# Kernel optimization log

Hardware: AMD Instinct MI355X
Metric: run time of the kernel (lower is better)

The kernel has to match this reference:

```python
import jax, jax.numpy as jnp
import numpy as np

N = 100_000   # nodes
E = 1_600_000 # edges (COO, directed as given)
D = 128       # input feature dim
H = 128       # hidden dim
L = 3         # layers


def setup_inputs() -> dict:
    key = jax.random.key(0)
    ks = jax.random.split(key, 2 + 2 * L)
    x = jax.random.normal(ks[0], (N, D), dtype=jnp.float32)
    edge_index = jax.random.randint(ks[1], (2, E), 0, N, dtype=jnp.int32)
    inp = {"x": x, "edge_index": edge_index}
    dims = [(D, H), (H, H), (H, H)]
    for i, (fi, fo) in enumerate(dims):
        scale = 1.0 / np.sqrt(fi)
        inp[f"W{i}"] = jax.random.uniform(ks[2 + 2 * i], (fi, fo), jnp.float32, -scale, scale)
        inp[f"b{i}"] = jax.random.uniform(ks[3 + 2 * i], (fo,), jnp.float32, -scale, scale)
    return inp


def reference(x, edge_index, W0, b0, W1, b1, W2, b2):
    n = x.shape[0]
    src, dst = edge_index[0], edge_index[1]
    # GCNConv default: add self-loops, symmetric D^{-1/2}(A+I)D^{-1/2} normalization
    loop = jnp.arange(n, dtype=edge_index.dtype)
    src = jnp.concatenate([src, loop])
    dst = jnp.concatenate([dst, loop])
    ones = jnp.ones(src.shape[0], dtype=x.dtype)
    deg = jax.ops.segment_sum(ones, dst, num_segments=n)          # [N]
    dinv = jnp.where(deg > 0, jax.lax.rsqrt(deg), 0.0)            # deg^{-1/2}, inf->0
    norm = dinv[src] * dinv[dst]                                  # [E+N]

    def gcn_conv(h, W, b):
        h = h @ W                                  # linear transform first (PyG order)
        msg = h[src] * norm[:, None]               # gather + scale, [E+N, H]
        return jax.ops.segment_sum(msg, dst, num_segments=n) + b

    for W, b in ((W0, b0), (W1, b1), (W2, b2)):
        x = jax.nn.relu(gcn_conv(x, W, b))
    return x
```

## Files before the change

kernel.cpp:

```cpp
#include <hip/hip_runtime.h>
#include <hip/hip_bf16.h>

#define TPB 256

typedef short s8v __attribute__((ext_vector_type(8)));
typedef float f4v __attribute__((ext_vector_type(4)));
typedef _Float16 h8v __attribute__((ext_vector_type(8)));

#define PB 128
#define BSHIFT 10
#define BSPAN 1024
#define PCHUNK 4096
#define WBLK 192
#define CAP 20480

__device__ __forceinline__ void split_f16(float v, _Float16& hi, _Float16& lo) {
    hi = (_Float16)v;
    lo = (_Float16)(v - (float)hi);
}


__global__ __launch_bounds__(256) void prep_kernel(const int* __restrict__ src,
                                                   const int* __restrict__ dst, int E,
                                                   int* __restrict__ bcursor,
                                                   unsigned int* __restrict__ part,
                                                   const float* __restrict__ W0,
                                                   const float* __restrict__ W1,
                                                   const float* __restrict__ W2,
                                                   unsigned short* __restrict__ Whi,
                                                   unsigned short* __restrict__ Wlo) {
    __shared__ int h[PB];
    __shared__ int gofs[PB];
    int t = threadIdx.x;
    if (blockIdx.x < WBLK) {
        int idx0 = blockIdx.x * 256 + t;
        if (idx0 < 3 * 16384) {
            int layer = idx0 >> 14;
            int e = idx0 & 16383;
            int k = e >> 7, ncol = e & 127;
            const float* W = (layer == 0) ? W0 : (layer == 1) ? W1 : W2;
            _Float16 hi, lo;
            split_f16(W[e], hi, lo);
            int ct = ncol >> 4;
            int lane = (((k >> 3) & 3) << 4) | (ncol & 15);
            int kki = k >> 5;
            int j = k & 7;
            int oidx = layer * 16384 + (((ct * 4 + kki) * 64 + lane) * 8 + j);
            ((_Float16*)Whi)[oidx] = hi;
            ((_Float16*)Wlo)[oidx] = lo;
        }
        return;
    }
    long base = (long)(blockIdx.x - WBLK) * PCHUNK;
    int cnt = (int)min((long)PCHUNK, (long)E - base);

    if (t < PB) h[t] = 0;
    __syncthreads();
    for (int j = t; j < cnt; j += 256)
        atomicAdd(&h[dst[base + j] >> BSHIFT], 1);
    __syncthreads();
    if (t < PB) {
        int c = h[t];
        int resv = (c > 0) ? atomicAdd(&bcursor[t], c) : 0;
        if (resv > CAP) resv = CAP;
        gofs[t] = t * CAP + resv;
    }
    __syncthreads();
    if (t < PB) h[t] = 0;
    __syncthreads();
    for (int j = t; j < cnt; j += 256) {
        int s = src[base + j], d = dst[base + j];
        int b = d >> BSHIFT;
        int idx = atomicAdd(&h[b], 1);
        long w = (long)gofs[b] + idx;
        long lim = (long)(b + 1) * CAP;
        if (w >= lim) w = lim - 1;
        part[w] = (unsigned int)s | ((unsigned int)(d & (BSPAN - 1)) << 17);
    }
}


__global__ __launch_bounds__(1024) void csr_kernel(const unsigned int* __restrict__ part,
                                                   const int* __restrict__ bcursor,
                                                   int* __restrict__ row, float* __restrict__ dinv,
                                                   int* __restrict__ esrc, int n, int E) {
    __shared__ int deg[BSPAN];
    __shared__ int lrow[BSPAN];
    __shared__ int cur[BSPAN];
    __shared__ int wsum[16];
    __shared__ int sbase[PB];
    __shared__ int wtot2[2];
    int b = blockIdx.x;
    int n0 = b << BSHIFT;
    int nn = min(BSPAN, n - n0);
    if (nn <= 0) return;
    int t = threadIdx.x;
    int lane = t & 63, wid = t >> 6;

    int szb = 0, v0 = 0;
    if (t < PB) {
        szb = min(bcursor[t], CAP);
        v0 = szb;
        for (int off = 1; off < 64; off <<= 1) {
            int u = __shfl_up(v0, off);
            if (lane >= off) v0 += u;
        }
        if (lane == 63) wtot2[wid] = v0;
    }
    __syncthreads();
    if (t < PB) {
        if (wid == 1) v0 += wtot2[0];
        sbase[t] = v0 - szb;
    }
    if (b == 0 && t == 0) row[n] = E;
    __syncthreads();
    int e0g = sbase[b];
    int size = min(bcursor[b], CAP);
    long pb0 = (long)b * CAP;

    deg[t] = 0;
    __syncthreads();
    for (int e = t; e < size; e += 1024)
        atomicAdd(&deg[part[pb0 + e] >> 17], 1);
    __syncthreads();

    int a = deg[t];
    int v = a;
    for (int off = 1; off < 64; off <<= 1) {
        int u = __shfl_up(v, off);
        if (lane >= off) v += u;
    }
    if (lane == 63) wsum[wid] = v;
    __syncthreads();
    if (wid == 0 && lane < 16) {
        int w = wsum[lane];
        for (int off = 1; off < 16; off <<= 1) {
            int u = __shfl_up(w, off);
            if (lane >= off) w += u;
        }
        wsum[lane] = w;
    }
    __syncthreads();
    int excl = v - a + ((wid > 0) ? wsum[wid - 1] : 0);
    lrow[t] = excl;
    cur[t] = 0;
    if (t < nn) {
        row[n0 + t] = e0g + excl;
        dinv[n0 + t] = rsqrtf((float)(deg[t] + 1));
    }
    __syncthreads();

    for (int e = t; e < size; e += 1024) {
        unsigned int p = part[pb0 + e];
        int d = p >> 17;
        int idx = atomicAdd(&cur[d], 1);
        esrc[e0g + lrow[d] + idx] = (int)(p & 0x1FFFFu);
    }
}


__global__ __launch_bounds__(256, 3) void gemm0_mfma(const float* __restrict__ Xf,
                                                     const unsigned short* __restrict__ Whs,
                                                     const unsigned short* __restrict__ Wls,
                                                     const float* __restrict__ dinv,
                                                     _Float16* __restrict__ Ch, int n) {
    __shared__ _Float16 Oh[128 * 136];
    int t = threadIdx.x;
    int wave = t >> 6, lane = t & 63;
    int ch = wave & 1, rh = wave >> 1;
    int lm = lane & 15, q = lane >> 4;
    long row0 = (long)blockIdx.x * 128 + rh * 64;

    const h8v* Wh8 = (const h8v*)Whs;
    const h8v* Wl8 = (const h8v*)Wls;

    float scs[4];
#pragma unroll
    for (int rt = 0; rt < 4; rt++) {
        long r = row0 + rt * 16 + lm;
        long rc = (r < n) ? r : (n - 1);
        scs[rt] = dinv[rc];
    }

    f4v acc[4][4];
#pragma unroll
    for (int rt = 0; rt < 4; rt++)
#pragma unroll
        for (int ct = 0; ct < 4; ct++) acc[rt][ct] = (f4v)0.0f;

#pragma unroll
    for (int kki = 0; kki < 4; kki++) {
        h8v bh[4], bl[4];
#pragma unroll
        for (int ct = 0; ct < 4; ct++) {
            int idx = (((ch * 4 + ct) * 4 + kki) * 64) + lane;
            bh[ct] = Wh8[idx];
            bl[ct] = Wl8[idx];
        }
        h8v ah[4], al[4];
#pragma unroll
        for (int rt = 0; rt < 4; rt++) {
            long r = row0 + rt * 16 + lm;
            long rr = (r < n) ? r : (n - 1);
            const float4* xf4 = (const float4*)(Xf + rr * 128 + kki * 32 + q * 8);
            float4 u0 = xf4[0], u1 = xf4[1];
            float uf[8] = {u0.x, u0.y, u0.z, u0.w, u1.x, u1.y, u1.z, u1.w};
            float sc = scs[rt];
            h8v hv, lv;
#pragma unroll
            for (int j = 0; j < 8; j++) {
                _Float16 hh, ll;
                split_f16(uf[j] * sc, hh, ll);
                hv[j] = hh; lv[j] = ll;
            }
            ah[rt] = hv; al[rt] = lv;
        }
#pragma unroll
        for (int rt = 0; rt < 4; rt++)
#pragma unroll
            for (int ct = 0; ct < 4; ct++) {
                acc[rt][ct] = __builtin_amdgcn_mfma_f32_16x16x32_f16(ah[rt], bh[ct], acc[rt][ct], 0, 0, 0);
                acc[rt][ct] = __builtin_amdgcn_mfma_f32_16x16x32_f16(ah[rt], bl[ct], acc[rt][ct], 0, 0, 0);
                acc[rt][ct] = __builtin_amdgcn_mfma_f32_16x16x32_f16(al[rt], bh[ct], acc[rt][ct], 0, 0, 0);
            }
    }

#pragma unroll
    for (int rt = 0; rt < 4; rt++)
#pragma unroll
        for (int reg = 0; reg < 4; reg++) {
            int lr = rh * 64 + rt * 16 + q * 4 + reg;
#pragma unroll
            for (int ct = 0; ct < 4; ct++)
                Oh[lr * 136 + ch * 64 + ct * 16 + lm] = (_Float16)acc[rt][ct][reg];
        }
    __syncthreads();

    long rowb = (long)blockIdx.x * 128;
    int lr = t >> 1;
    int cb = (t & 1) * 64;
    if (rowb + lr < n) {
        const uint4* s = (const uint4*)&Oh[lr * 136 + cb];
        uint4* d = (uint4*)&Ch[(rowb + lr) * 128 + cb];
#pragma unroll
        for (int u = 0; u < 8; u++) d[u] = s[u];
    }
}


__global__ __launch_bounds__(256) void fused_kernel(const h8v* __restrict__ hIn,
                                                    const float* __restrict__ dinv,
                                                    const int* __restrict__ row,
                                                    const int* __restrict__ esrc,
                                                    const float* __restrict__ bias,
                                                    const unsigned short* __restrict__ Whs,
                                                    const unsigned short* __restrict__ Wls,
                                                    _Float16* __restrict__ hOut, int n, int nzr) {
    __shared__ _Float16 Ah[16 * 136];
    __shared__ _Float16 Al[16 * 136];
    int t = threadIdx.x;
    int g = t >> 4, lane = t & 15;
    long i = (long)blockIdx.x * 16 + g;

    float one = 1.0f;
    asm("" : "+v"(one));

    h8v hv, lv;
    if (i < n) {
        float di = dinv[i];
        h8v self = hIn[i * 16 + lane];
        float acc[8];
#pragma unroll
        for (int k = 0; k < 8; k++) acc[k] = (float)self[k];

        int e0 = row[i], e1 = row[i + 1];
        int deg = e1 - e0;
        int eFull = e1 - (deg & 7);
        int e = e0;
        for (; e < eFull; e += 8) {
            int s[8];
#pragma unroll
            for (int j = 0; j < 8; j++) s[j] = esrc[e + j];
            h8v v[8];
#pragma unroll
            for (int j = 0; j < 8; j++) v[j] = hIn[(size_t)s[j] * 16 + lane];
#pragma unroll
            for (int j = 0; j < 8; j++)
#pragma unroll
                for (int k = 0; k < 8; k++) acc[k] = fmaf((float)v[j][k], one, acc[k]);
        }
        if (e < e1) {
            int s[8];
#pragma unroll
            for (int j = 0; j < 8; j++) {
                int idx = e + j;
                int ic = (idx < e1) ? idx : (e1 - 1);
                int sv = esrc[ic];
                s[j] = (idx < e1) ? sv : nzr;
            }
            h8v v[8];
#pragma unroll
            for (int j = 0; j < 8; j++) v[j] = hIn[(size_t)s[j] * 16 + lane];
#pragma unroll
            for (int j = 0; j < 8; j++)
#pragma unroll
                for (int k = 0; k < 8; k++) acc[k] = fmaf((float)v[j][k], one, acc[k]);
        }

        const float4* b4 = (const float4*)(bias + lane * 8);
        float4 bA = b4[0], bB = b4[1];
        float bb[8] = {bA.x, bA.y, bA.z, bA.w, bB.x, bB.y, bB.z, bB.w};
#pragma unroll
        for (int k = 0; k < 8; k++) {
            float r = di * fmaxf(di * acc[k] + bb[k], 0.f);
            _Float16 hh, ll;
            split_f16(r, hh, ll);
            hv[k] = hh; lv[k] = ll;
        }
    } else {
#pragma unroll
        for (int k = 0; k < 8; k++) { hv[k] = (_Float16)0.f; lv[k] = (_Float16)0.f; }
    }

    *(h8v*)&Ah[g * 136 + lane * 8] = hv;
    *(h8v*)&Al[g * 136 + lane * 8] = lv;
    __syncthreads();

    int w = t >> 6, l64 = t & 63;
    int lm = l64 & 15, q = l64 >> 4;

    const h8v* Wh8 = (const h8v*)Whs;
    const h8v* Wl8 = (const h8v*)Wls;
    h8v Bh[2][4], Bl[2][4];
#pragma unroll
    for (int c = 0; c < 2; c++)
#pragma unroll
        for (int kki = 0; kki < 4; kki++) {
            int idx = (((w * 2 + c) * 4 + kki) * 64) + l64;
            Bh[c][kki] = Wh8[idx];
            Bl[c][kki] = Wl8[idx];
        }

    f4v acc2[2];
    acc2[0] = (f4v)0.0f; acc2[1] = (f4v)0.0f;

#pragma unroll
    for (int kki = 0; kki < 4; kki++) {
        h8v ah = *(const h8v*)&Ah[lm * 136 + kki * 32 + q * 8];
        h8v al = *(const h8v*)&Al[lm * 136 + kki * 32 + q * 8];
#pragma unroll
        for (int c = 0; c < 2; c++) {
            acc2[c] = __builtin_amdgcn_mfma_f32_16x16x32_f16(ah, Bh[c][kki], acc2[c], 0, 0, 0);
            acc2[c] = __builtin_amdgcn_mfma_f32_16x16x32_f16(ah, Bl[c][kki], acc2[c], 0, 0, 0);
            acc2[c] = __builtin_amdgcn_mfma_f32_16x16x32_f16(al, Bh[c][kki], acc2[c], 0, 0, 0);
        }
    }
    __syncthreads();

    _Float16* Oh = (_Float16*)Ah;
#pragma unroll
    for (int c = 0; c < 2; c++)
#pragma unroll
        for (int reg = 0; reg < 4; reg++)
            Oh[(q * 4 + reg) * 136 + (w * 2 + c) * 16 + lm] = (_Float16)acc2[c][reg];
    __syncthreads();

    long gi = (long)blockIdx.x * 16 + (t >> 4);
    if (gi < n) {
        uint4 v = *(const uint4*)&Oh[(t >> 4) * 136 + (t & 15) * 8];
        *(uint4*)&hOut[gi * 128 + (size_t)(t & 15) * 8] = v;
    }
}


__global__ __launch_bounds__(256) void agg_final(const h8v* __restrict__ hH,
                                                 const float* __restrict__ dinv,
                                                 const int* __restrict__ row,
                                                 const int* __restrict__ esrc,
                                                 const float* __restrict__ bias,
                                                 float* __restrict__ out, int n, int nzr) {
    int g    = threadIdx.x >> 4;
    int lane = threadIdx.x & 15;
    int i = blockIdx.x * 16 + g;
    if (i >= n) return;

    float one = 1.0f;
    asm("" : "+v"(one));

    float di = dinv[i];
    h8v self = hH[(size_t)i * 16 + lane];
    float acc[8];
#pragma unroll
    for (int k = 0; k < 8; k++) acc[k] = (float)self[k];

    int e0 = row[i], e1 = row[i + 1];
    int deg = e1 - e0;
    int eFull = e1 - (deg & 7);
    int e = e0;
    for (; e < eFull; e += 8) {
        int s[8];
#pragma unroll
        for (int j = 0; j < 8; j++) s[j] = esrc[e + j];
        h8v v[8];
#pragma unroll
        for (int j = 0; j < 8; j++) v[j] = hH[(size_t)s[j] * 16 + lane];
#pragma unroll
        for (int j = 0; j < 8; j++)
#pragma unroll
            for (int k = 0; k < 8; k++) acc[k] = fmaf((float)v[j][k], one, acc[k]);
    }
    if (e < e1) {
        int s[8];
#pragma unroll
        for (int j = 0; j < 8; j++) {
            int idx = e + j;
            int ic = (idx < e1) ? idx : (e1 - 1);
            int sv = esrc[ic];
            s[j] = (idx < e1) ? sv : nzr;
        }
        h8v v[8];
#pragma unroll
        for (int j = 0; j < 8; j++) v[j] = hH[(size_t)s[j] * 16 + lane];
#pragma unroll
        for (int j = 0; j < 8; j++)
#pragma unroll
            for (int k = 0; k < 8; k++) acc[k] = fmaf((float)v[j][k], one, acc[k]);
    }

    const float4* b4 = (const float4*)(bias + lane * 8);
    float4 bA = b4[0], bB = b4[1];
    float4* o4 = (float4*)(out + (size_t)i * 128 + lane * 8);
    o4[0] = make_float4(fmaxf(di * acc[0] + bA.x, 0.f), fmaxf(di * acc[1] + bA.y, 0.f),
                        fmaxf(di * acc[2] + bA.z, 0.f), fmaxf(di * acc[3] + bA.w, 0.f));
    o4[1] = make_float4(fmaxf(di * acc[4] + bB.x, 0.f), fmaxf(di * acc[5] + bB.y, 0.f),
                        fmaxf(di * acc[6] + bB.z, 0.f), fmaxf(di * acc[7] + bB.w, 0.f));
}


extern "C" void kernel_launch(void* const* d_in, const int* in_sizes, int n_in,
                              void* d_out, int out_size, void* d_ws, size_t ws_size,
                              hipStream_t stream) {
    const float* x  = (const float*)d_in[0];
    const int*   ei = (const int*)d_in[1];
    const float* W0 = (const float*)d_in[2];
    const float* b0 = (const float*)d_in[3];
    const float* W1 = (const float*)d_in[4];
    const float* b1 = (const float*)d_in[5];
    const float* W2 = (const float*)d_in[6];
    const float* b2 = (const float*)d_in[7];

    const int H = 128;
    int n = in_sizes[0] / H;
    int E = in_sizes[1] / 2;
    const int* srcp = ei;
    const int* dstp = ei + E;

    int gemm_blocks = (n + 127) / 128;
    long npad = (long)gemm_blocks * 128;
    long rowsAlloc = npad + 128;
    int nbuck = (n + BSPAN - 1) >> BSHIFT;
    int nchunk = (E + PCHUNK - 1) / PCHUNK;

    char* p = (char*)d_ws;
    auto alloc = [&](size_t bytes) {
        void* r = (void*)p;
        p += (bytes + 255) & ~(size_t)255;
        return r;
    };
    _Float16* bufH0 = (_Float16*)alloc((size_t)rowsAlloc * H * 2);
    _Float16* bufH1 = (_Float16*)alloc((size_t)rowsAlloc * H * 2);
    unsigned short* Whs = (unsigned short*)alloc(3 * 16384 * 2);
    unsigned short* Wls = (unsigned short*)alloc(3 * 16384 * 2);
    float* dinv  = (float*)alloc((size_t)n * sizeof(float));
    int*  row    = (int*)alloc((size_t)(n + 1) * sizeof(int));
    int*  bcursor= (int*)alloc(PB * sizeof(int));
    unsigned int* part = (unsigned int*)alloc((size_t)PB * CAP * 4);
    int*  esrc   = (int*)alloc((size_t)E * sizeof(int));

    hipMemsetAsync(bcursor, 0, PB * sizeof(int), stream);
    hipMemsetAsync(esrc, 0, (size_t)E * sizeof(int), stream);
    hipMemsetAsync(bufH0 + (size_t)n * H, 0, (size_t)(rowsAlloc - n) * H * 2, stream);
    hipMemsetAsync(bufH1 + (size_t)n * H, 0, (size_t)(rowsAlloc - n) * H * 2, stream);

    prep_kernel<<<WBLK + nchunk, 256, 0, stream>>>(srcp, dstp, E, bcursor, part,
                                                   W0, W1, W2, Whs, Wls);
    csr_kernel<<<nbuck, 1024, 0, stream>>>(part, bcursor, row, dinv, esrc, n, E);

    float* out = (float*)d_out;
    int node_blocks = (n + 15) / 16;

    gemm0_mfma<<<gemm_blocks, 256, 0, stream>>>(x, Whs, Wls, dinv, bufH0, n);
    fused_kernel<<<node_blocks, 256, 0, stream>>>((const h8v*)bufH0, dinv, row, esrc, b0,
                                                  Whs + 16384, Wls + 16384, bufH1, n, n);
    fused_kernel<<<node_blocks, 256, 0, stream>>>((const h8v*)bufH1, dinv, row, esrc, b1,
                                                  Whs + 32768, Wls + 32768, bufH0, n, n);
    agg_final<<<node_blocks, 256, 0, stream>>>((const h8v*)bufH0, dinv, row, esrc, b2, out, n, n);
}
```

Baseline: 373.5 us.

## Reorder nodes by in-degree to balance per-block aggregation work

Builds an in-degree histogram during CSR construction, scans it in descending order, and scatters node ids into a permutation so nodes of similar degree are processed together. The fused aggregation+GEMM kernels and the final aggregation read through this permutation to pick their nodes and scatter outputs. The aim is less intra-wave and intra-block imbalance from varying edge counts. It costs two extra small kernel launches, a contended global atomic histogram, and irregular output writes and self-row reads caused by the permuted node order.

```diff
diff --git a/kernel.cpp b/kernel.cpp
--- a/kernel.cpp
+++ b/kernel.cpp
@@ -13,6 +13,7 @@
 #define PCHUNK 4096
 #define WBLK 192
 #define CAP 20480
+#define DBINS 256
 
 __device__ __forceinline__ void split_f16(float v, _Float16& hi, _Float16& lo) {
     hi = (_Float16)v;
@@ -83,7 +84,8 @@
 __global__ __launch_bounds__(1024) void csr_kernel(const unsigned int* __restrict__ part,
                                                    const int* __restrict__ bcursor,
                                                    int* __restrict__ row, float* __restrict__ dinv,
-                                                   int* __restrict__ esrc, int n, int E) {
+                                                   int* __restrict__ esrc, int* __restrict__ dhist,
+                                                   int n, int E) {
     __shared__ int deg[BSPAN];
     __shared__ int lrow[BSPAN];
     __shared__ int cur[BSPAN];
@@ -147,6 +149,7 @@
     if (t < nn) {
         row[n0 + t] = e0g + excl;
         dinv[n0 + t] = rsqrtf((float)(deg[t] + 1));
+        atomicAdd(&dhist[min(deg[t], DBINS - 1)], 1);
     }
     __syncthreads();
 
@@ -155,6 +158,27 @@
         int d = p >> 17;
         int idx = atomicAdd(&cur[d], 1);
         esrc[e0g + lrow[d] + idx] = (int)(p & 0x1FFFFu);
+    }
+}
+
+
+__global__ void dscan_kernel(const int* __restrict__ dhist, int* __restrict__ dbase) {
+    if (threadIdx.x == 0) {
+        int acc = 0;
+        for (int b = DBINS - 1; b >= 0; --b) { dbase[b] = acc; acc += dhist[b]; }
+    }
+}
+
+__global__ __launch_bounds__(256) void dscatter_kernel(const int* __restrict__ row,
+                                                       const int* __restrict__ dbase,
+                                                       int* __restrict__ dcursor,
+                                                       int* __restrict__ perm, int n) {
+    int i = blockIdx.x * 256 + threadIdx.x;
+    if (i < n) {
+        int deg = row[i + 1] - row[i];
+        int b = min(deg, DBINS - 1);
+        int pos = atomicAdd(&dcursor[b], 1);
+        perm[dbase[b] + pos] = i;
     }
 }
 
@@ -252,6 +276,7 @@
                                                     const float* __restrict__ dinv,
                                                     const int* __restrict__ row,
                                                     const int* __restrict__ esrc,
+                                                    const int* __restrict__ perm,
                                                     const float* __restrict__ bias,
                                                     const unsigned short* __restrict__ Whs,
                                                     const unsigned short* __restrict__ Wls,
@@ -260,13 +285,14 @@
     __shared__ _Float16 Al[16 * 136];
     int t = threadIdx.x;
     int g = t >> 4, lane = t & 15;
-    long i = (long)blockIdx.x * 16 + g;
+    int pidx = blockIdx.x * 16 + g;
 
     float one = 1.0f;
     asm("" : "+v"(one));
 
     h8v hv, lv;
-    if (i < n) {
+    if (pidx < n) {
+        long i = perm[pidx];
         float di = dinv[i];
         h8v self = hIn[i * 16 + lane];
         float acc[8];
@@ -365,8 +391,9 @@
             Oh[(q * 4 + reg) * 136 + (w * 2 + c) * 16 + lm] = (_Float16)acc2[c][reg];
     __syncthreads();
 
-    long gi = (long)blockIdx.x * 16 + (t >> 4);
-    if (gi < n) {
+    int oidx = blockIdx.x * 16 + (t >> 4);
+    if (oidx < n) {
+        long gi = perm[oidx];
         uint4 v = *(const uint4*)&Oh[(t >> 4) * 136 + (t & 15) * 8];
         *(uint4*)&hOut[gi * 128 + (size_t)(t & 15) * 8] = v;
     }
@@ -377,12 +404,14 @@
                                                  const float* __restrict__ dinv,
                                                  const int* __restrict__ row,
                                                  const int* __restrict__ esrc,
+                                                 const int* __restrict__ perm,
                                                  const float* __restrict__ bias,
                                                  float* __restrict__ out, int n, int nzr) {
     int g    = threadIdx.x >> 4;
     int lane = threadIdx.x & 15;
-    int i = blockIdx.x * 16 + g;
-    if (i >= n) return;
+    int pidx = blockIdx.x * 16 + g;
+    if (pidx >= n) return;
+    long i = perm[pidx];
 
     float one = 1.0f;
     asm("" : "+v"(one));
@@ -474,25 +503,33 @@
     float* dinv  = (float*)alloc((size_t)n * sizeof(float));
     int*  row    = (int*)alloc((size_t)(n + 1) * sizeof(int));
     int*  bcursor= (int*)alloc(PB * sizeof(int));
+    int*  dhist  = (int*)alloc(DBINS * sizeof(int));
+    int*  dbase  = (int*)alloc(DBINS * sizeof(int));
+    int*  dcursor= (int*)alloc(DBINS * sizeof(int));
+    int*  perm   = (int*)alloc((size_t)n * sizeof(int));
     unsigned int* part = (unsigned int*)alloc((size_t)PB * CAP * 4);
     int*  esrc   = (int*)alloc((size_t)E * sizeof(int));
 
     hipMemsetAsync(bcursor, 0, PB * sizeof(int), stream);
+    hipMemsetAsync(dhist, 0, 2 * DBINS * sizeof(int), stream);
+    hipMemsetAsync(dcursor, 0, DBINS * sizeof(int), stream);
     hipMemsetAsync(esrc, 0, (size_t)E * sizeof(int), stream);
     hipMemsetAsync(bufH0 + (size_t)n * H, 0, (size_t)(rowsAlloc - n) * H * 2, stream);
     hipMemsetAsync(bufH1 + (size_t)n * H, 0, (size_t)(rowsAlloc - n) * H * 2, stream);
 
     prep_kernel<<<WBLK + nchunk, 256, 0, stream>>>(srcp, dstp, E, bcursor, part,
                                                    W0, W1, W2, Whs, Wls);
-    csr_kernel<<<nbuck, 1024, 0, stream>>>(part, bcursor, row, dinv, esrc, n, E);
+    csr_kernel<<<nbuck, 1024, 0, stream>>>(part, bcursor, row, dinv, esrc, dhist, n, E);
+    dscan_kernel<<<1, 64, 0, stream>>>(dhist, dbase);
+    dscatter_kernel<<<(n + 255) / 256, 256, 0, stream>>>(row, dbase, dcursor, perm, n);
 
     float* out = (float*)d_out;
     int node_blocks = (n + 15) / 16;
 
     gemm0_mfma<<<gemm_blocks, 256, 0, stream>>>(x, Whs, Wls, dinv, bufH0, n);
-    fused_kernel<<<node_blocks, 256, 0, stream>>>((const h8v*)bufH0, dinv, row, esrc, b0,
+    fused_kernel<<<node_blocks, 256, 0, stream>>>((const h8v*)bufH0, dinv, row, esrc, perm, b0,
                                                   Whs + 16384, Wls + 16384, bufH1, n, n);
-    fused_kernel<<<node_blocks, 256, 0, stream>>>((const h8v*)bufH1, dinv, row, esrc, b1,
+    fused_kernel<<<node_blocks, 256, 0, stream>>>((const h8v*)bufH1, dinv, row, esrc, perm, b1,
                                                   Whs + 32768, Wls + 32768, bufH0, n, n);
-    agg_final<<<node_blocks, 256, 0, stream>>>((const h8v*)bufH0, dinv, row, esrc, b2, out, n, n);
-}
+    agg_final<<<node_blocks, 256, 0, stream>>>((const h8v*)bufH0, dinv, row, esrc, perm, b2, out, n, n);
+}
```

Measured after the change: 904.3 us. 142% more time.

## Replace bucketed CSR build with global degree count, scan, and atomic scatter

Applied to the files above, without the earlier changes.

The two-pass bucket partition (prep plus csr_kernel with local shared-memory sorting) is replaced by three steps. First, per-node in-degrees are counted with global atomics, together with per-bucket totals. Second, a per-bucket scan produces row offsets, dinv and per-node cursors. Third, a scatter kernel places each edge source through a global atomicAdd on its destination's cursor. This removes the intermediate partition buffer and its capacity clamp, but adds many contended global atomics and random writes to esrc. It also makes the order of neighbours within a row nondeterministic, which can change the floating-point summation order.

```diff
diff --git a/kernel.cpp b/kernel.cpp
--- a/kernel.cpp
+++ b/kernel.cpp
@@ -12,7 +12,6 @@
 #define BSPAN 1024
 #define PCHUNK 4096
 #define WBLK 192
-#define CAP 20480
 
 __device__ __forceinline__ void split_f16(float v, _Float16& hi, _Float16& lo) {
     hi = (_Float16)v;
@@ -20,17 +19,15 @@
 }
 
 
-__global__ __launch_bounds__(256) void prep_kernel(const int* __restrict__ src,
-                                                   const int* __restrict__ dst, int E,
-                                                   int* __restrict__ bcursor,
-                                                   unsigned int* __restrict__ part,
-                                                   const float* __restrict__ W0,
-                                                   const float* __restrict__ W1,
-                                                   const float* __restrict__ W2,
-                                                   unsigned short* __restrict__ Whi,
-                                                   unsigned short* __restrict__ Wlo) {
+__global__ __launch_bounds__(256) void degcnt_kernel(const int* __restrict__ dst, int E,
+                                                     int* __restrict__ deg,
+                                                     int* __restrict__ bsize,
+                                                     const float* __restrict__ W0,
+                                                     const float* __restrict__ W1,
+                                                     const float* __restrict__ W2,
+                                                     unsigned short* __restrict__ Whi,
+                                                     unsigned short* __restrict__ Wlo) {
     __shared__ int h[PB];
-    __shared__ int gofs[PB];
     int t = threadIdx.x;
     if (blockIdx.x < WBLK) {
         int idx0 = blockIdx.x * 256 + t;
@@ -56,37 +53,21 @@
 
     if (t < PB) h[t] = 0;
     __syncthreads();
-    for (int j = t; j < cnt; j += 256)
-        atomicAdd(&h[dst[base + j] >> BSHIFT], 1);
-    __syncthreads();
-    if (t < PB) {
-        int c = h[t];
-        int resv = (c > 0) ? atomicAdd(&bcursor[t], c) : 0;
-        if (resv > CAP) resv = CAP;
-        gofs[t] = t * CAP + resv;
-    }
-    __syncthreads();
-    if (t < PB) h[t] = 0;
-    __syncthreads();
     for (int j = t; j < cnt; j += 256) {
-        int s = src[base + j], d = dst[base + j];
-        int b = d >> BSHIFT;
-        int idx = atomicAdd(&h[b], 1);
-        long w = (long)gofs[b] + idx;
-        long lim = (long)(b + 1) * CAP;
-        if (w >= lim) w = lim - 1;
-        part[w] = (unsigned int)s | ((unsigned int)(d & (BSPAN - 1)) << 17);
-    }
-}
-
-
-__global__ __launch_bounds__(1024) void csr_kernel(const unsigned int* __restrict__ part,
-                                                   const int* __restrict__ bcursor,
-                                                   int* __restrict__ row, float* __restrict__ dinv,
-                                                   int* __restrict__ esrc, int n, int E) {
-    __shared__ int deg[BSPAN];
-    __shared__ int lrow[BSPAN];
-    __shared__ int cur[BSPAN];
+        int d = dst[base + j];
+        atomicAdd(&deg[d], 1);
+        atomicAdd(&h[d >> BSHIFT], 1);
+    }
+    __syncthreads();
+    if (t < PB && h[t] > 0) atomicAdd(&bsize[t], h[t]);
+}
+
+
+__global__ __launch_bounds__(1024) void rowscan_kernel(const int* __restrict__ deg,
+                                                       const int* __restrict__ bsize,
+                                                       int* __restrict__ row,
+                                                       float* __restrict__ dinv,
+                                                       int* __restrict__ cursor, int n, int E) {
     __shared__ int wsum[16];
     __shared__ int sbase[PB];
     __shared__ int wtot2[2];
@@ -99,7 +80,7 @@
 
     int szb = 0, v0 = 0;
     if (t < PB) {
-        szb = min(bcursor[t], CAP);
+        szb = bsize[t];
         v0 = szb;
         for (int off = 1; off < 64; off <<= 1) {
             int u = __shfl_up(v0, off);
@@ -115,16 +96,8 @@
     if (b == 0 && t == 0) row[n] = E;
     __syncthreads();
     int e0g = sbase[b];
-    int size = min(bcursor[b], CAP);
-    long pb0 = (long)b * CAP;
-
-    deg[t] = 0;
-    __syncthreads();
-    for (int e = t; e < size; e += 1024)
-        atomicAdd(&deg[part[pb0 + e] >> 17], 1);
-    __syncthreads();
-
-    int a = deg[t];
+
+    int a = (t < nn) ? deg[n0 + t] : 0;
     int v = a;
     for (int off = 1; off < 64; off <<= 1) {
         int u = __shfl_up(v, off);
@@ -142,19 +115,24 @@
     }
     __syncthreads();
     int excl = v - a + ((wid > 0) ? wsum[wid - 1] : 0);
-    lrow[t] = excl;
-    cur[t] = 0;
     if (t < nn) {
-        row[n0 + t] = e0g + excl;
-        dinv[n0 + t] = rsqrtf((float)(deg[t] + 1));
-    }
-    __syncthreads();
-
-    for (int e = t; e < size; e += 1024) {
-        unsigned int p = part[pb0 + e];
-        int d = p >> 17;
-        int idx = atomicAdd(&cur[d], 1);
-        esrc[e0g + lrow[d] + idx] = (int)(p & 0x1FFFFu);
+        int base = e0g + excl;
+        row[n0 + t] = base;
+        cursor[n0 + t] = base;
+        dinv[n0 + t] = rsqrtf((float)(a + 1));
+    }
+}
+
+
+__global__ __launch_bounds__(256) void scatter_kernel(const int* __restrict__ src,
+                                                      const int* __restrict__ dst, int E,
+                                                      int* __restrict__ cursor,
+                                                      int* __restrict__ esrc) {
+    int stride = gridDim.x * 256;
+    for (int e = blockIdx.x * 256 + threadIdx.x; e < E; e += stride) {
+        int s = src[e], d = dst[e];
+        int pos = atomicAdd(&cursor[d], 1);
+        esrc[pos] = s;
     }
 }
 
@@ -473,18 +451,21 @@
     unsigned short* Wls = (unsigned short*)alloc(3 * 16384 * 2);
     float* dinv  = (float*)alloc((size_t)n * sizeof(float));
     int*  row    = (int*)alloc((size_t)(n + 1) * sizeof(int));
-    int*  bcursor= (int*)alloc(PB * sizeof(int));
-    unsigned int* part = (unsigned int*)alloc((size_t)PB * CAP * 4);
+    int*  deg    = (int*)alloc((size_t)n * sizeof(int));
+    int*  cursor = (int*)alloc((size_t)n * sizeof(int));
+    int*  bsize  = (int*)alloc(PB * sizeof(int));
     int*  esrc   = (int*)alloc((size_t)E * sizeof(int));
 
-    hipMemsetAsync(bcursor, 0, PB * sizeof(int), stream);
+    hipMemsetAsync(deg, 0, (size_t)n * sizeof(int), stream);
+    hipMemsetAsync(bsize, 0, PB * sizeof(int), stream);
     hipMemsetAsync(esrc, 0, (size_t)E * sizeof(int), stream);
     hipMemsetAsync(bufH0 + (size_t)n * H, 0, (size_t)(rowsAlloc - n) * H * 2, stream);
     hipMemsetAsync(bufH1 + (size_t)n * H, 0, (size_t)(rowsAlloc - n) * H * 2, stream);
 
-    prep_kernel<<<WBLK + nchunk, 256, 0, stream>>>(srcp, dstp, E, bcursor, part,
-                                                   W0, W1, W2, Whs, Wls);
-    csr_kernel<<<nbuck, 1024, 0, stream>>>(part, bcursor, row, dinv, esrc, n, E);
+    degcnt_kernel<<<WBLK + nchunk, 256, 0, stream>>>(dstp, E, deg, bsize,
+                                                     W0, W1, W2, Whs, Wls);
+    rowscan_kernel<<<nbuck, 1024, 0, stream>>>(deg, bsize, row, dinv, cursor, n, E);
+    scatter_kernel<<<2048, 256, 0, stream>>>(srcp, dstp, E, cursor, esrc);
 
     float* out = (float*)d_out;
     int node_blocks = (n + 15) / 16;
```

Measured after the change: 543.3 us. 45.5% more time.
